# Performance work log

Measured on AMD Instinct MI355X. Metric: run time of the kernel, lower is better.

Reference implementation:

```python
import jax, jax.numpy as jnp
import numpy as np

N = 100000
E = 1600000
H = 128
L = 3


def setup_inputs() -> dict:
    key = jax.random.key(0)
    ks = jax.random.split(key, 8)
    z = jax.random.normal(ks[0], (N, H), dtype=jnp.float32)
    edge_index = jax.random.randint(ks[1], (2, E), 0, N, dtype=jnp.int64)
    edge_weight = jax.random.uniform(ks[2], (E,), dtype=jnp.float32)
    s = 1.0 / np.sqrt(H)
    weight = jax.random.uniform(ks[3], (L, H, H), minval=-s, maxval=s, dtype=jnp.float32)
    w_ih = jax.random.uniform(ks[4], (3 * H, H), minval=-s, maxval=s, dtype=jnp.float32)
    w_hh = jax.random.uniform(ks[5], (3 * H, H), minval=-s, maxval=s, dtype=jnp.float32)
    b_ih = jax.random.uniform(ks[6], (3 * H,), minval=-s, maxval=s, dtype=jnp.float32)
    b_hh = jax.random.uniform(ks[7], (3 * H,), minval=-s, maxval=s, dtype=jnp.float32)
    return {"z": z, "edge_weight": edge_weight, "weight": weight,
            "w_ih": w_ih, "w_hh": w_hh, "b_ih": b_ih, "b_hh": b_hh,
            "edge_index": edge_index}


def _gru_cell(m, h, w_ih, w_hh, b_ih, b_hh):
    # torch GRUCell: gate order (r, z, n)
    gi = m @ w_ih.T + b_ih   # [N, 3H]
    gh = h @ w_hh.T + b_hh   # [N, 3H]
    i_r, i_z, i_n = jnp.split(gi, 3, axis=-1)
    h_r, h_z, h_n = jnp.split(gh, 3, axis=-1)
    r = jax.nn.sigmoid(i_r + h_r)
    zg = jax.nn.sigmoid(i_z + h_z)
    n = jnp.tanh(i_n + r * h_n)
    return (1.0 - zg) * n + zg * h


def reference(z, edge_weight, weight, w_ih, w_hh, b_ih, b_hh, edge_index):
    src = edge_index[0]  # x_j gathered from source nodes
    dst = edge_index[1]  # aggregated at target nodes
    x = z  # in_channels == out_channels, so no zero padding needed
    for l in range(L):
        m = x @ weight[l]                                  # [N, H]
        msg = m[src] * edge_weight[:, None]                # [E, H]
        agg = jax.ops.segment_sum(msg, dst, num_segments=N)  # aggr='add'
        x = _gru_cell(agg, x, w_ih, w_hh, b_ih, b_hh)
    return x
```

## Files before the change

kernel.cpp:

```cpp
#include <hip/hip_runtime.h>

typedef __bf16 bf16x8 __attribute__((ext_vector_type(8)));
typedef float floatx4 __attribute__((ext_vector_type(4)));

#define NPB 256
#define NPB_SHIFT 8
#define MAXNB 1024
#define TILE 4096

static __device__ __forceinline__ float bfu_to_f(unsigned short u) {
    unsigned int x = ((unsigned int)u) << 16;
    return __builtin_bit_cast(float, x);
}
static __device__ __forceinline__ unsigned short f_to_bfu(float f) {
    unsigned int u = __builtin_bit_cast(unsigned int, f);
    unsigned int r = (u + 0x7fffu + ((u >> 16) & 1u)) >> 16;
    return (unsigned short)r;
}

__global__ void detect_k(const unsigned short* __restrict__ bih_u,
                         const unsigned int* __restrict__ ei_u,
                         int* __restrict__ flags) {
    if (threadIdx.x == 0 && blockIdx.x == 0) {
        int votes = 0;
        for (int i = 0; i < 64; i++) {
            unsigned short u = bih_u[2 * i];
            unsigned int ex = (u >> 7) & 0xFF;
            if (ex >= 64 && ex < 124) votes++;
        }
        flags[0] = (votes >= 48) ? 1 : 0;
        int zeros = 0;
        for (int i = 0; i < 64; i++) {
            if (ei_u[2 * i + 1] == 0u) zeros++;
        }
        flags[1] = (zeros == 64) ? 1 : 0;
    }
}


__global__ void cvt_bf16_k(const void* __restrict__ in, unsigned short* __restrict__ out,
                           int n, const int* __restrict__ flags) {
    int i = blockIdx.x * 256 + threadIdx.x;
    if (i >= n) return;
    if (flags[0]) out[i] = ((const unsigned short*)in)[i];
    else out[i] = f_to_bfu(((const float*)in)[i]);
}

__global__ void cvt_bias_k(const void* __restrict__ bih, const void* __restrict__ bhh,
                           float* __restrict__ bih_f, float* __restrict__ bhh_f,
                           const int* __restrict__ flags) {
    int i = blockIdx.x * 256 + threadIdx.x;
    if (i >= 768) return;
    const void* src = (i < 384) ? bih : bhh;
    int j = (i < 384) ? i : i - 384;
    float v = flags[0] ? bfu_to_f(((const unsigned short*)src)[j]) : ((const float*)src)[j];
    if (i < 384) bih_f[j] = v;
    else bhh_f[j] = v;
}

__global__ void out_k(const unsigned short* __restrict__ xb, void* __restrict__ out,
                      int n, const int* __restrict__ flags) {
    int i = blockIdx.x * 256 + threadIdx.x;
    if (i >= n) return;
    if (flags[0]) ((unsigned short*)out)[i] = xb[i];
    else ((float*)out)[i] = bfu_to_f(xb[i]);
}


static __device__ __forceinline__ int load_idx(const unsigned int* eiu, size_t pos, int is64) {
    return (int)eiu[is64 ? 2 * pos : pos];
}

__global__ __launch_bounds__(256) void count_k(const unsigned int* __restrict__ eiu,
                                               int* __restrict__ bucketCnt, int E,
                                               const int* __restrict__ flags) {
    __shared__ int cnt[MAXNB];
    int t = threadIdx.x;
    for (int b = t; b < MAXNB; b += 256) cnt[b] = 0;
    __syncthreads();
    int is64 = flags[1];
    int e0 = blockIdx.x * TILE;
    int e1 = min(e0 + TILE, E);
    for (int e = e0 + t; e < e1; e += 256) {
        int d = load_idx(eiu, (size_t)E + e, is64);
        atomicAdd(&cnt[d >> NPB_SHIFT], 1);
    }
    __syncthreads();
    for (int b = t; b < MAXNB; b += 256) {
        int c = cnt[b];
        if (c) atomicAdd(&bucketCnt[b], c);
    }
}

__global__ void scanB_k(const int* __restrict__ bucketCnt, int* __restrict__ bucketBase,
                        int* __restrict__ bucketCursor, int NB, int E) {
    __shared__ int sh[MAXNB];
    int t = threadIdx.x;
    int v = (t < NB) ? bucketCnt[t] : 0;
    sh[t] = v;
    __syncthreads();
    for (int off = 1; off < MAXNB; off <<= 1) {
        int u = (t >= off) ? sh[t - off] : 0;
        __syncthreads();
        sh[t] += u;
        __syncthreads();
    }
    if (t < NB) {
        int b = sh[t] - v;
        bucketBase[t] = b;
        bucketCursor[t] = b;
    }
    if (t == 0) bucketBase[NB] = E;
}

__global__ __launch_bounds__(256) void bin_k(const unsigned int* __restrict__ eiu,
                                             const void* __restrict__ ew,
                                             int* __restrict__ bucketCursor,
                                             uint2* __restrict__ rec8,
                                             int* __restrict__ dstA, int E,
                                             const int* __restrict__ flags) {
    __shared__ int cnt[MAXNB];
    __shared__ int basel[MAXNB];
    int t = threadIdx.x;
    for (int b = t; b < MAXNB; b += 256) cnt[b] = 0;
    __syncthreads();
    int is64 = flags[1];
    int isb = flags[0];
    int e0 = blockIdx.x * TILE;
    int e1 = min(e0 + TILE, E);
    for (int e = e0 + t; e < e1; e += 256) {
        int d = load_idx(eiu, (size_t)E + e, is64);
        atomicAdd(&cnt[d >> NPB_SHIFT], 1);
    }
    __syncthreads();
    for (int b = t; b < MAXNB; b += 256) {
        int c = cnt[b];
        basel[b] = c ? atomicAdd(&bucketCursor[b], c) : 0;
        cnt[b] = 0;
    }
    __syncthreads();
    for (int e = e0 + t; e < e1; e += 256) {
        int s = load_idx(eiu, (size_t)e, is64);
        int d = load_idx(eiu, (size_t)E + e, is64);
        float w = isb ? bfu_to_f(((const unsigned short*)ew)[e]) : ((const float*)ew)[e];
        int b = d >> NPB_SHIFT;
        int p = basel[b] + atomicAdd(&cnt[b], 1);
        dstA[p] = d;
        rec8[p] = make_uint2((unsigned int)s, __builtin_bit_cast(unsigned int, w));
    }
}

__global__ __launch_bounds__(256) void csr_k(const uint2* __restrict__ rec8,
                                             const int* __restrict__ dstA,
                                             const int* __restrict__ bucketBase,
                                             int* __restrict__ offsets,
                                             uint2* __restrict__ rec, int N, int E) {
    __shared__ int cnt[NPB];
    __shared__ int sh[NPB];
    __shared__ int cur[NPB];
    int t = threadIdx.x;
    int b = blockIdx.x;
    int n0 = b << NPB_SHIFT;
    int nodes = min(NPB, N - n0);
    int ebase = bucketBase[b];
    int ecnt = bucketBase[b + 1] - ebase;

    cnt[t] = 0;
    __syncthreads();
    for (int i = t; i < ecnt; i += 256) {
        int d = dstA[ebase + i] - n0;
        atomicAdd(&cnt[d], 1);
    }
    __syncthreads();
    int v = cnt[t];
    sh[t] = v;
    __syncthreads();
    for (int off = 1; off < NPB; off <<= 1) {
        int u = (t >= off) ? sh[t - off] : 0;
        __syncthreads();
        sh[t] += u;
        __syncthreads();
    }
    int loff = sh[t] - v;
    if (t < nodes) offsets[n0 + t] = ebase + loff;
    cur[t] = ebase + loff;
    if (b == 0 && t == 0) offsets[N] = E;
    __syncthreads();
    for (int i = t; i < ecnt; i += 256) {
        int d = dstA[ebase + i] - n0;
        int p = atomicAdd(&cur[d], 1);
        rec[p] = rec8[ebase + i];
    }
}


static __device__ __forceinline__ float dot8_bf(uint4 wv, uint4 iv) {
    float s;
    s  = bfu_to_f((unsigned short)(wv.x)) * bfu_to_f((unsigned short)(iv.x));
    s += bfu_to_f((unsigned short)(wv.x >> 16)) * bfu_to_f((unsigned short)(iv.x >> 16));
    s += bfu_to_f((unsigned short)(wv.y)) * bfu_to_f((unsigned short)(iv.y));
    s += bfu_to_f((unsigned short)(wv.y >> 16)) * bfu_to_f((unsigned short)(iv.y >> 16));
    s += bfu_to_f((unsigned short)(wv.z)) * bfu_to_f((unsigned short)(iv.z));
    s += bfu_to_f((unsigned short)(wv.z >> 16)) * bfu_to_f((unsigned short)(iv.z >> 16));
    s += bfu_to_f((unsigned short)(wv.w)) * bfu_to_f((unsigned short)(iv.w));
    s += bfu_to_f((unsigned short)(wv.w >> 16)) * bfu_to_f((unsigned short)(iv.w >> 16));
    return s;
}

__global__ void make_ut_k(const void* __restrict__ weight, const void* __restrict__ wih,
                          unsigned short* __restrict__ Ut, const int* __restrict__ flags) {
    int idx = blockIdx.x * 256 + threadIdx.x;
    if (idx >= 3 * 384 * 128) return;
    int isb = flags[0];
    int a = idx & 127;
    int j = (idx >> 7) % 384;
    int l = idx / (384 * 128);
    float s = 0.f;
    if (isb) {
        const uint4* W4 = (const uint4*)((const unsigned short*)weight + (size_t)l * 16384 + a * 128);
        const uint4* I4 = (const uint4*)((const unsigned short*)wih + (size_t)j * 128);
#pragma unroll
        for (int c = 0; c < 16; c++) s += dot8_bf(W4[c], I4[c]);
    } else {
        const float4* W4 = (const float4*)((const float*)weight + (size_t)l * 16384 + a * 128);
        const float4* I4 = (const float4*)((const float*)wih + (size_t)j * 128);
#pragma unroll
        for (int c = 0; c < 32; c++) {
            float4 w = W4[c], i = I4[c];
            s += w.x * i.x + w.y * i.y + w.z * i.z + w.w * i.w;
        }
    }
    Ut[idx] = f_to_bfu(s);
}

__global__ void pack_b_k(const unsigned short* __restrict__ Ut,
                         const void* __restrict__ whh,
                         unsigned short* __restrict__ Bp,
                         const int* __restrict__ flags) {
    int idx = blockIdx.x * 256 + threadIdx.x;
    if (idx >= 3 * 4 * 12 * 4 * 64) return;
    int lane = idx & 63;
    int kc = (idx >> 6) & 3;
    int rest = idx >> 8;
    int j = rest % 12;
    int cg = (rest / 12) & 3;
    int l = rest / 48;
    int s = j / 6;
    int g = (j % 6) >> 1;
    int t = j & 1;
    int col = (cg * 2 + t) * 16 + (lane & 15);
    int k = kc * 32 + (lane >> 4) * 8;
    (void)g;
    unsigned short tmp[8];
    const unsigned short* src;
    if (s == 0) {
        int row384 = (j % 6) >> 1;
        row384 = row384 * 128 + col;
        src = Ut + (size_t)l * 49152 + row384 * 128 + k;
    } else if (flags[0]) {
        int row384 = ((j % 6) >> 1) * 128 + col;
        src = (const unsigned short*)whh + (size_t)row384 * 128 + k;
    } else {
        int row384 = ((j % 6) >> 1) * 128 + col;
        const float* wf = (const float*)whh + (size_t)row384 * 128 + k;
        for (int i = 0; i < 8; i++) tmp[i] = f_to_bfu(wf[i]);
        src = tmp;
    }
    unsigned short* dst = Bp + (size_t)l * 98304 + (((size_t)(cg * 12 + j) * 4 + kc) * 64 + lane) * 8;
    for (int i = 0; i < 8; i++) dst[i] = src[i];
}


__global__ __launch_bounds__(256) void agg_k(const unsigned short* __restrict__ xb,
                                             const int* __restrict__ offs,
                                             const uint2* __restrict__ rec,
                                             unsigned short* __restrict__ y, int N) {
    int node = (int)((blockIdx.x * 256 + threadIdx.x) >> 4);
    int l16 = threadIdx.x & 15;
    if (node >= N) return;
    int b = offs[node];
    int e2 = offs[node + 1];
    const uint4* xp4 = (const uint4*)xb;
    float a0[8], a1[8];
#pragma unroll
    for (int i = 0; i < 8; i++) { a0[i] = 0.f; a1[i] = 0.f; }

    auto fma_row = [&](float* acc, uint4 v, float w) {
        acc[0] += w * __builtin_bit_cast(float, v.x << 16);
        acc[1] += w * __builtin_bit_cast(float, v.x & 0xffff0000u);
        acc[2] += w * __builtin_bit_cast(float, v.y << 16);
        acc[3] += w * __builtin_bit_cast(float, v.y & 0xffff0000u);
        acc[4] += w * __builtin_bit_cast(float, v.z << 16);
        acc[5] += w * __builtin_bit_cast(float, v.z & 0xffff0000u);
        acc[6] += w * __builtin_bit_cast(float, v.w << 16);
        acc[7] += w * __builtin_bit_cast(float, v.w & 0xffff0000u);
    };

    int e = b;
    for (; e + 4 <= e2; e += 4) {
        uint2 r0 = rec[e], r1 = rec[e + 1], r2 = rec[e + 2], r3 = rec[e + 3];
        uint4 v0 = xp4[(size_t)r0.x * 16 + l16];
        uint4 v1 = xp4[(size_t)r1.x * 16 + l16];
        uint4 v2 = xp4[(size_t)r2.x * 16 + l16];
        uint4 v3 = xp4[(size_t)r3.x * 16 + l16];
        fma_row(a0, v0, __builtin_bit_cast(float, r0.y));
        fma_row(a1, v1, __builtin_bit_cast(float, r1.y));
        fma_row(a0, v2, __builtin_bit_cast(float, r2.y));
        fma_row(a1, v3, __builtin_bit_cast(float, r3.y));
    }
    for (; e < e2; e++) {
        uint2 r = rec[e];
        uint4 v = xp4[(size_t)r.x * 16 + l16];
        fma_row(a0, v, __builtin_bit_cast(float, r.y));
    }

    uint4 o;
    o.x = (unsigned int)f_to_bfu(a0[0] + a1[0]) | ((unsigned int)f_to_bfu(a0[1] + a1[1]) << 16);
    o.y = (unsigned int)f_to_bfu(a0[2] + a1[2]) | ((unsigned int)f_to_bfu(a0[3] + a1[3]) << 16);
    o.z = (unsigned int)f_to_bfu(a0[4] + a1[4]) | ((unsigned int)f_to_bfu(a0[5] + a1[5]) << 16);
    o.w = (unsigned int)f_to_bfu(a0[6] + a1[6]) | ((unsigned int)f_to_bfu(a0[7] + a1[7]) << 16);
    ((uint4*)y)[(size_t)node * 16 + l16] = o;
}


__global__ __launch_bounds__(512, 6) void gru_k(const unsigned short* __restrict__ y,
                                                const unsigned short* __restrict__ xin,
                                                unsigned short* __restrict__ xout,
                                                const unsigned short* __restrict__ Bp,
                                                const float* __restrict__ bih,
                                                const float* __restrict__ bhh, int N) {
    __shared__ uint4 Blds[3072];

    int bid = blockIdx.x;
    int r8 = bid & 7;
    int inner = bid >> 3;
    int cg = inner & 3;
    int rb = ((inner >> 2) << 3) + r8;
    int row0 = rb << 7;
    if (row0 >= N) return;

    int tid = threadIdx.x;
    int wave = tid >> 6;
    int wc = wave & 1;
    int wr = wave >> 1;
    int lane = tid & 63;
    int quad = lane >> 4;
    int m16 = lane & 15;

    {
        const uint4* bsrc = (const uint4*)(Bp + (size_t)cg * 24576);
#pragma unroll
        for (int i = 0; i < 6; i++) Blds[tid + i * 512] = bsrc[tid + i * 512];
    }
    __syncthreads();

    floatx4 acc[2][4];
#pragma unroll
    for (int rt = 0; rt < 2; rt++)
#pragma unroll
        for (int s = 0; s < 4; s++) acc[rt][s] = (floatx4){0.f, 0.f, 0.f, 0.f};

    int rA[2];
#pragma unroll
    for (int rt = 0; rt < 2; rt++) {
        int r = row0 + wr * 32 + rt * 16 + m16;
        rA[rt] = (r < N) ? r : N - 1;
    }

    const unsigned short* bl = (const unsigned short*)Blds;

#pragma unroll
    for (int kc = 0; kc < 4; kc++) {
        int ko = kc * 32 + quad * 8;
        bf16x8 aY[2], aX[2];
#pragma unroll
        for (int rt = 0; rt < 2; rt++) {
            aY[rt] = *(const bf16x8*)(y + (size_t)rA[rt] * 128 + ko);
            aX[rt] = *(const bf16x8*)(xin + (size_t)rA[rt] * 128 + ko);
        }
        bf16x8 bU[3], bW[3];
#pragma unroll
        for (int g = 0; g < 3; g++) {
            int jU = g * 2 + wc;
            int jW = 6 + g * 2 + wc;
            bU[g] = *(const bf16x8*)(bl + ((size_t)(jU * 4 + kc) * 64 + lane) * 8);
            bW[g] = *(const bf16x8*)(bl + ((size_t)(jW * 4 + kc) * 64 + lane) * 8);
        }
#pragma unroll
        for (int rt = 0; rt < 2; rt++) {
            acc[rt][0] = __builtin_amdgcn_mfma_f32_16x16x32_bf16(aY[rt], bU[0], acc[rt][0], 0, 0, 0);
            acc[rt][0] = __builtin_amdgcn_mfma_f32_16x16x32_bf16(aX[rt], bW[0], acc[rt][0], 0, 0, 0);
            acc[rt][1] = __builtin_amdgcn_mfma_f32_16x16x32_bf16(aY[rt], bU[1], acc[rt][1], 0, 0, 0);
            acc[rt][1] = __builtin_amdgcn_mfma_f32_16x16x32_bf16(aX[rt], bW[1], acc[rt][1], 0, 0, 0);
            acc[rt][2] = __builtin_amdgcn_mfma_f32_16x16x32_bf16(aY[rt], bU[2], acc[rt][2], 0, 0, 0);
            acc[rt][3] = __builtin_amdgcn_mfma_f32_16x16x32_bf16(aX[rt], bW[2], acc[rt][3], 0, 0, 0);
        }
    }

    int ch = cg * 32 + wc * 16 + m16;
    float b_r = bih[ch] + bhh[ch];
    float b_z = bih[128 + ch] + bhh[128 + ch];
    float bi_n = bih[256 + ch];
    float bh_n = bhh[256 + ch];
#pragma unroll
    for (int rt = 0; rt < 2; rt++) {
#pragma unroll
        for (int ri = 0; ri < 4; ri++) {
            int row = row0 + wr * 32 + rt * 16 + quad * 4 + ri;
            if (row >= N) continue;
            float sr = acc[rt][0][ri] + b_r;
            float sz = acc[rt][1][ri] + b_z;
            float gn = acc[rt][2][ri] + bi_n;
            float hn = acc[rt][3][ri] + bh_n;
            float r = __builtin_amdgcn_rcpf(1.f + __expf(-sr));
            float zg = __builtin_amdgcn_rcpf(1.f + __expf(-sz));
            float x2 = gn + r * hn;
            float n = 1.f - 2.f * __builtin_amdgcn_rcpf(1.f + __expf(2.f * x2));
            float h = bfu_to_f(xin[(size_t)row * 128 + ch]);
            float o = n + zg * (h - n);
            xout[(size_t)row * 128 + ch] = f_to_bfu(o);
        }
    }
}


extern "C" void kernel_launch(void* const* d_in, const int* in_sizes, int n_in,
                              void* d_out, int out_size, void* d_ws, size_t ws_size,
                              hipStream_t stream) {
    const int N = in_sizes[0] / 128;
    const int E = in_sizes[1];
    const int NB = (N + NPB - 1) >> NPB_SHIFT;

    const void* z = d_in[0];
    const void* ew = d_in[1];
    const void* weight = d_in[2];
    const void* wih = d_in[3];
    const void* whh = d_in[4];
    const void* bih = d_in[5];
    const void* bhh = d_in[6];
    const unsigned int* eiu = (const unsigned int*)d_in[7];

    unsigned short* y = (unsigned short*)d_out;

    size_t off = 0;
    char* base = (char*)d_ws;
    auto carve = [&](size_t bytes) -> void* {
        void* p = base + off;
        off = (off + bytes + 255) & ~(size_t)255;
        return p;
    };
    unsigned short* xb = (unsigned short*)carve((size_t)N * 128 * 2);
    unsigned short* xb2 = (unsigned short*)carve((size_t)N * 128 * 2);
    uint2* rec8 = (uint2*)carve((size_t)E * 8);
    int* dstA = (int*)carve((size_t)E * 4);
    uint2* rec = (uint2*)carve((size_t)E * 8);
    int* offsets = (int*)carve((size_t)(N + 1) * 4);
    int* bucketCnt = (int*)carve(MAXNB * 4);
    int* bucketBase = (int*)carve((MAXNB + 1) * 4);
    int* bucketCursor = (int*)carve(MAXNB * 4);
    unsigned short* Ut = (unsigned short*)carve((size_t)3 * 384 * 128 * 2);
    unsigned short* Bp = (unsigned short*)carve((size_t)3 * 48 * 4 * 64 * 8 * 2);
    float* bih_f = (float*)carve(384 * 4);
    float* bhh_f = (float*)carve(384 * 4);
    int* flags = (int*)carve(256);

    detect_k<<<1, 64, 0, stream>>>((const unsigned short*)bih, eiu, flags);

    cvt_bf16_k<<<(N * 128 + 255) / 256, 256, 0, stream>>>(z, xb, N * 128, flags);
    cvt_bias_k<<<3, 256, 0, stream>>>(bih, bhh, bih_f, bhh_f, flags);

    hipMemsetAsync(bucketCnt, 0, MAXNB * 4, stream);
    int gbin = (E + TILE - 1) / TILE;
    count_k<<<gbin, 256, 0, stream>>>(eiu, bucketCnt, E, flags);
    scanB_k<<<1, MAXNB, 0, stream>>>(bucketCnt, bucketBase, bucketCursor, NB, E);
    bin_k<<<gbin, 256, 0, stream>>>(eiu, ew, bucketCursor, rec8, dstA, E, flags);
    csr_k<<<NB, NPB, 0, stream>>>(rec8, dstA, bucketBase, offsets, rec, N, E);

    make_ut_k<<<(3 * 384 * 128 + 255) / 256, 256, 0, stream>>>(weight, wih, Ut, flags);
    pack_b_k<<<(3 * 4 * 12 * 4 * 64 + 255) / 256, 256, 0, stream>>>(Ut, whh, Bp, flags);

    const int RB = (N + 127) >> 7;
    const int grid_gru = 8 * ((RB + 7) >> 3) * 4;

    const unsigned short* cur = xb;
    unsigned short* nxt = xb2;
    for (int l = 0; l < 3; l++) {
        agg_k<<<(N + 15) / 16, 256, 0, stream>>>(cur, offsets, rec, y, N);
        gru_k<<<grid_gru, 512, 0, stream>>>(y, cur, nxt, Bp + (size_t)l * 98304,
                                            bih_f, bhh_f, N);
        const unsigned short* tmp = cur;
        cur = nxt;
        nxt = (unsigned short*)tmp;
    }

    out_k<<<(N * 128 + 255) / 256, 256, 0, stream>>>(cur, d_out, N * 128, flags);
}
```

Measured before the change: 652.5 us.

## Make GRU kernel persistent with fixed grid looping over row blocks per XCD

The GRU gate kernel now launches a fixed grid of 512 blocks. Each block loads its packed weight slice into LDS once and loops over several 128-row blocks inside a contiguous per-XCD range, instead of launching one block per row block and reloading weights every time. The inner loop now loads all four K chunks of y first and runs the U MFMAs, then does the same for x with the W MFMAs, which exposes more loads per wave at the cost of more registers (launch bounds occupancy drops from 6 to 4). The detect kernel is also parallelised across 64 threads with shared atomics, and pack_b_k has a small index cleanup.

```diff
diff --git a/kernel.cpp b/kernel.cpp
--- a/kernel.cpp
+++ b/kernel.cpp
@@ -21,19 +21,18 @@
 __global__ void detect_k(const unsigned short* __restrict__ bih_u,
                          const unsigned int* __restrict__ ei_u,
                          int* __restrict__ flags) {
-    if (threadIdx.x == 0 && blockIdx.x == 0) {
-        int votes = 0;
-        for (int i = 0; i < 64; i++) {
-            unsigned short u = bih_u[2 * i];
-            unsigned int ex = (u >> 7) & 0xFF;
-            if (ex >= 64 && ex < 124) votes++;
-        }
-        flags[0] = (votes >= 48) ? 1 : 0;
-        int zeros = 0;
-        for (int i = 0; i < 64; i++) {
-            if (ei_u[2 * i + 1] == 0u) zeros++;
-        }
-        flags[1] = (zeros == 64) ? 1 : 0;
+    __shared__ int sv, sz;
+    int t = threadIdx.x;
+    if (t == 0) { sv = 0; sz = 0; }
+    __syncthreads();
+    unsigned short u = bih_u[2 * t];
+    unsigned int ex = (u >> 7) & 0xFF;
+    if (ex >= 64 && ex < 124) atomicAdd(&sv, 1);
+    if (ei_u[2 * t + 1] == 0u) atomicAdd(&sz, 1);
+    __syncthreads();
+    if (t == 0) {
+        flags[0] = (sv >= 48) ? 1 : 0;
+        flags[1] = (sz == 64) ? 1 : 0;
     }
 }
 
@@ -250,18 +249,14 @@
     int t = j & 1;
     int col = (cg * 2 + t) * 16 + (lane & 15);
     int k = kc * 32 + (lane >> 4) * 8;
-    (void)g;
+    int row384 = g * 128 + col;
     unsigned short tmp[8];
     const unsigned short* src;
     if (s == 0) {
-        int row384 = (j % 6) >> 1;
-        row384 = row384 * 128 + col;
         src = Ut + (size_t)l * 49152 + row384 * 128 + k;
     } else if (flags[0]) {
-        int row384 = ((j % 6) >> 1) * 128 + col;
         src = (const unsigned short*)whh + (size_t)row384 * 128 + k;
     } else {
-        int row384 = ((j % 6) >> 1) * 128 + col;
         const float* wf = (const float*)whh + (size_t)row384 * 128 + k;
         for (int i = 0; i < 8; i++) tmp[i] = f_to_bfu(wf[i]);
         src = tmp;
@@ -323,102 +318,113 @@
 }
 
 
-__global__ __launch_bounds__(512, 6) void gru_k(const unsigned short* __restrict__ y,
+__global__ __launch_bounds__(512, 4) void gru_k(const unsigned short* __restrict__ y,
                                                 const unsigned short* __restrict__ xin,
                                                 unsigned short* __restrict__ xout,
                                                 const unsigned short* __restrict__ Bp,
                                                 const float* __restrict__ bih,
-                                                const float* __restrict__ bhh, int N) {
+                                                const float* __restrict__ bhh,
+                                                int N, int RB, int PR) {
     __shared__ uint4 Blds[3072];
 
     int bid = blockIdx.x;
-    int r8 = bid & 7;
-    int inner = bid >> 3;
-    int cg = inner & 3;
-    int rb = ((inner >> 2) << 3) + r8;
-    int row0 = rb << 7;
-    if (row0 >= N) return;
+    int xcd = bid & 7;
+    int slot = bid >> 3;
+    int cg = slot & 3;
+    int rslot = slot >> 2;
 
     int tid = threadIdx.x;
+    {
+        const uint4* bsrc = (const uint4*)(Bp + (size_t)cg * 24576);
+#pragma unroll
+        for (int i = 0; i < 6; i++) Blds[tid + i * 512] = bsrc[tid + i * 512];
+    }
+    __syncthreads();
+
     int wave = tid >> 6;
     int wc = wave & 1;
     int wr = wave >> 1;
     int lane = tid & 63;
     int quad = lane >> 4;
     int m16 = lane & 15;
-
-    {
-        const uint4* bsrc = (const uint4*)(Bp + (size_t)cg * 24576);
-#pragma unroll
-        for (int i = 0; i < 6; i++) Blds[tid + i * 512] = bsrc[tid + i * 512];
-    }
-    __syncthreads();
-
-    floatx4 acc[2][4];
-#pragma unroll
-    for (int rt = 0; rt < 2; rt++)
-#pragma unroll
-        for (int s = 0; s < 4; s++) acc[rt][s] = (floatx4){0.f, 0.f, 0.f, 0.f};
-
-    int rA[2];
-#pragma unroll
-    for (int rt = 0; rt < 2; rt++) {
-        int r = row0 + wr * 32 + rt * 16 + m16;
-        rA[rt] = (r < N) ? r : N - 1;
-    }
-
     const unsigned short* bl = (const unsigned short*)Blds;
-
-#pragma unroll
-    for (int kc = 0; kc < 4; kc++) {
-        int ko = kc * 32 + quad * 8;
-        bf16x8 aY[2], aX[2];
-#pragma unroll
-        for (int rt = 0; rt < 2; rt++) {
-            aY[rt] = *(const bf16x8*)(y + (size_t)rA[rt] * 128 + ko);
-            aX[rt] = *(const bf16x8*)(xin + (size_t)rA[rt] * 128 + ko);
-        }
-        bf16x8 bU[3], bW[3];
-#pragma unroll
-        for (int g = 0; g < 3; g++) {
-            int jU = g * 2 + wc;
-            int jW = 6 + g * 2 + wc;
-            bU[g] = *(const bf16x8*)(bl + ((size_t)(jU * 4 + kc) * 64 + lane) * 8);
-            bW[g] = *(const bf16x8*)(bl + ((size_t)(jW * 4 + kc) * 64 + lane) * 8);
-        }
-#pragma unroll
-        for (int rt = 0; rt < 2; rt++) {
-            acc[rt][0] = __builtin_amdgcn_mfma_f32_16x16x32_bf16(aY[rt], bU[0], acc[rt][0], 0, 0, 0);
-            acc[rt][0] = __builtin_amdgcn_mfma_f32_16x16x32_bf16(aX[rt], bW[0], acc[rt][0], 0, 0, 0);
-            acc[rt][1] = __builtin_amdgcn_mfma_f32_16x16x32_bf16(aY[rt], bU[1], acc[rt][1], 0, 0, 0);
-            acc[rt][1] = __builtin_amdgcn_mfma_f32_16x16x32_bf16(aX[rt], bW[1], acc[rt][1], 0, 0, 0);
-            acc[rt][2] = __builtin_amdgcn_mfma_f32_16x16x32_bf16(aY[rt], bU[2], acc[rt][2], 0, 0, 0);
-            acc[rt][3] = __builtin_amdgcn_mfma_f32_16x16x32_bf16(aX[rt], bW[2], acc[rt][3], 0, 0, 0);
-        }
-    }
 
     int ch = cg * 32 + wc * 16 + m16;
     float b_r = bih[ch] + bhh[ch];
     float b_z = bih[128 + ch] + bhh[128 + ch];
     float bi_n = bih[256 + ch];
     float bh_n = bhh[256 + ch];
-#pragma unroll
-    for (int rt = 0; rt < 2; rt++) {
-#pragma unroll
-        for (int ri = 0; ri < 4; ri++) {
-            int row = row0 + wr * 32 + rt * 16 + quad * 4 + ri;
-            if (row >= N) continue;
-            float sr = acc[rt][0][ri] + b_r;
-            float sz = acc[rt][1][ri] + b_z;
-            float gn = acc[rt][2][ri] + bi_n;
-            float hn = acc[rt][3][ri] + bh_n;
-            float r = __builtin_amdgcn_rcpf(1.f + __expf(-sr));
-            float zg = __builtin_amdgcn_rcpf(1.f + __expf(-sz));
-            float x2 = gn + r * hn;
-            float n = 1.f - 2.f * __builtin_amdgcn_rcpf(1.f + __expf(2.f * x2));
-            float h = bfu_to_f(xin[(size_t)row * 128 + ch]);
-            float o = n + zg * (h - n);
-            xout[(size_t)row * 128 + ch] = f_to_bfu(o);
+
+    int rbEnd = min((xcd + 1) * PR, RB);
+    for (int rb = xcd * PR + rslot; rb < rbEnd; rb += 16) {
+        int row0 = rb << 7;
+        int rA[2];
+#pragma unroll
+        for (int rt = 0; rt < 2; rt++) {
+            int r = row0 + wr * 32 + rt * 16 + m16;
+            rA[rt] = (r < N) ? r : N - 1;
+        }
+
+        floatx4 acc[2][4];
+#pragma unroll
+        for (int rt = 0; rt < 2; rt++)
+#pragma unroll
+            for (int s = 0; s < 4; s++) acc[rt][s] = (floatx4){0.f, 0.f, 0.f, 0.f};
+
+        bf16x8 a[2][4];
+
+#pragma unroll
+        for (int rt = 0; rt < 2; rt++)
+#pragma unroll
+            for (int kc = 0; kc < 4; kc++)
+                a[rt][kc] = *(const bf16x8*)(y + (size_t)rA[rt] * 128 + kc * 32 + quad * 8);
+#pragma unroll
+        for (int kc = 0; kc < 4; kc++) {
+#pragma unroll
+            for (int g = 0; g < 3; g++) {
+                int jU = g * 2 + wc;
+                bf16x8 b = *(const bf16x8*)(bl + ((size_t)(jU * 4 + kc) * 64 + lane) * 8);
+                int s = (g == 2) ? 2 : g;
+                acc[0][s] = __builtin_amdgcn_mfma_f32_16x16x32_bf16(a[0][kc], b, acc[0][s], 0, 0, 0);
+                acc[1][s] = __builtin_amdgcn_mfma_f32_16x16x32_bf16(a[1][kc], b, acc[1][s], 0, 0, 0);
+            }
+        }
+
+#pragma unroll
+        for (int rt = 0; rt < 2; rt++)
+#pragma unroll
+            for (int kc = 0; kc < 4; kc++)
+                a[rt][kc] = *(const bf16x8*)(xin + (size_t)rA[rt] * 128 + kc * 32 + quad * 8);
+#pragma unroll
+        for (int kc = 0; kc < 4; kc++) {
+#pragma unroll
+            for (int g = 0; g < 3; g++) {
+                int jW = 6 + g * 2 + wc;
+                bf16x8 b = *(const bf16x8*)(bl + ((size_t)(jW * 4 + kc) * 64 + lane) * 8);
+                int s = (g == 2) ? 3 : g;
+                acc[0][s] = __builtin_amdgcn_mfma_f32_16x16x32_bf16(a[0][kc], b, acc[0][s], 0, 0, 0);
+                acc[1][s] = __builtin_amdgcn_mfma_f32_16x16x32_bf16(a[1][kc], b, acc[1][s], 0, 0, 0);
+            }
+        }
+
+#pragma unroll
+        for (int rt = 0; rt < 2; rt++) {
+#pragma unroll
+            for (int ri = 0; ri < 4; ri++) {
+                int row = row0 + wr * 32 + rt * 16 + quad * 4 + ri;
+                if (row >= N) continue;
+                float sr = acc[rt][0][ri] + b_r;
+                float sz = acc[rt][1][ri] + b_z;
+                float gn = acc[rt][2][ri] + bi_n;
+                float hn = acc[rt][3][ri] + bh_n;
+                float r = __builtin_amdgcn_rcpf(1.f + __expf(-sr));
+                float zg = __builtin_amdgcn_rcpf(1.f + __expf(-sz));
+                float x2 = gn + r * hn;
+                float n = 1.f - 2.f * __builtin_amdgcn_rcpf(1.f + __expf(2.f * x2));
+                float h = bfu_to_f(xin[(size_t)row * 128 + ch]);
+                float o = n + zg * (h - n);
+                xout[(size_t)row * 128 + ch] = f_to_bfu(o);
+            }
         }
     }
 }
@@ -480,14 +486,14 @@
     pack_b_k<<<(3 * 4 * 12 * 4 * 64 + 255) / 256, 256, 0, stream>>>(Ut, whh, Bp, flags);
 
     const int RB = (N + 127) >> 7;
-    const int grid_gru = 8 * ((RB + 7) >> 3) * 4;
+    const int PR = (RB + 7) >> 3;
 
     const unsigned short* cur = xb;
     unsigned short* nxt = xb2;
     for (int l = 0; l < 3; l++) {
         agg_k<<<(N + 15) / 16, 256, 0, stream>>>(cur, offsets, rec, y, N);
-        gru_k<<<grid_gru, 512, 0, stream>>>(y, cur, nxt, Bp + (size_t)l * 98304,
-                                            bih_f, bhh_f, N);
+        gru_k<<<512, 512, 0, stream>>>(y, cur, nxt, Bp + (size_t)l * 98304,
+                                       bih_f, bhh_f, N, RB, PR);
         const unsigned short* tmp = cur;
         cur = nxt;
         nxt = (unsigned short*)tmp;
```

Measured after the change: 709.6 us. +8.8%, slower.
